# Kernel tuning notes

Measured on AMD Instinct MI355X. Metric: run time of the kernel, lower is better.

Reference implementation:

```python
import jax, jax.numpy as jnp
import numpy as np

B, N, C, H = 2, 2048, 256, 8
HD = C // H
EPS = 1e-5


def _cdist(a, b):
    # a: (B,N,D), b: (B,M,D) -> (B,N,M) euclidean distance (torch.cdist p=2)
    d2 = (jnp.sum(a * a, -1)[:, :, None] + jnp.sum(b * b, -1)[:, None, :]
          - 2.0 * jnp.einsum('bnd,bmd->bnm', a, b))
    return jnp.sqrt(jnp.maximum(d2, 0.0))


def _ln(x, g, b):
    # LayerNorm over last axis
    m = jnp.mean(x, -1, keepdims=True)
    v = jnp.var(x, -1, keepdims=True)
    return (x - m) / jnp.sqrt(v + EPS) * g + b


def _conv1d(x, w, b=None):
    # 1x1 Conv1d: x (B,Cin,N), w (Cout,Cin)
    y = jnp.einsum('oc,bcn->bon', w, x)
    return y if b is None else y + b[:, None]


def setup_inputs() -> dict:
    key = jax.random.key(0)
    ks = jax.random.split(key, 32)
    s = 0.05
    inp = {
        'xyz_A': jax.random.normal(ks[0], (B, N, 3), jnp.float32),
        'featA': jax.random.normal(ks[1], (B, C, N), jnp.float32),
        'xyz_B': jax.random.normal(ks[2], (B, N, 3), jnp.float32),
        'featB': jax.random.normal(ks[3], (B, C, N), jnp.float32),
        # q/k/v projections (Conv1d 1x1)
        'qw': jax.random.normal(ks[4], (C, C), jnp.float32) * s,
        'qb': jnp.zeros((C,), jnp.float32),
        'kw': jax.random.normal(ks[5], (C, C), jnp.float32) * s,
        'kb': jnp.zeros((C,), jnp.float32),
        'vw': jax.random.normal(ks[6], (C, C), jnp.float32) * s,
        'vb': jnp.zeros((C,), jnp.float32),
        # spatial_bias_mlp: Conv2d(1,H/2,1,bias=False) -> BN2d(eval) -> ReLU -> Conv2d(H/2,H,1)
        'sbw1': jax.random.normal(ks[7], (H // 2,), jnp.float32) * s,
        'sbg': jnp.ones((H // 2,), jnp.float32),
        'sbb': jnp.zeros((H // 2,), jnp.float32),
        'sbm': jax.random.normal(ks[8], (H // 2,), jnp.float32) * 0.1,
        'sbv': jax.random.uniform(ks[9], (H // 2,), jnp.float32, 0.5, 1.5),
        'sbw2': jax.random.normal(ks[10], (H, H // 2), jnp.float32) * s,
        'sbb2': jnp.zeros((H,), jnp.float32),
        # dissimilarity projections
        'qdw': jax.random.normal(ks[11], (C, C), jnp.float32) * s,
        'qdb': jnp.zeros((C,), jnp.float32),
        'kdw': jax.random.normal(ks[12], (C, C), jnp.float32) * s,
        'kdb': jnp.zeros((C,), jnp.float32),
        # LayerNorms
        'lin_g': jnp.ones((C,), jnp.float32), 'lin_b': jnp.zeros((C,), jnp.float32),
        'lsim_g': jnp.ones((C,), jnp.float32), 'lsim_b': jnp.zeros((C,), jnp.float32),
        'ldis_g': jnp.ones((C,), jnp.float32), 'ldis_b': jnp.zeros((C,), jnp.float32),
        # fusion MLP: Conv1d(3C,2C,bias=False) -> BN1d(eval) -> ReLU -> Dropout(eval) -> Conv1d(2C,C)
        'fw1': jax.random.normal(ks[13], (2 * C, 3 * C), jnp.float32) * s,
        'fbg': jnp.ones((2 * C,), jnp.float32),
        'fbb': jnp.zeros((2 * C,), jnp.float32),
        'fbm': jax.random.normal(ks[14], (2 * C,), jnp.float32) * 0.1,
        'fbv': jax.random.uniform(ks[15], (2 * C,), jnp.float32, 0.5, 1.5),
        'fw2': jax.random.normal(ks[16], (C, 2 * C), jnp.float32) * s,
        'fb2': jnp.zeros((C,), jnp.float32),
    }
    return inp


def _forward(xyz_A, featA, xyz_B, featB, qw, qb, kw, kb, vw, vb,
             sbw1, sbg, sbb, sbm, sbv, sbw2, sbb2,
             qdw, qdb, kdw, kdb,
             lin_g, lin_b, lsim_g, lsim_b, ldis_g, ldis_b,
             fw1, fbg, fbb, fbm, fbv, fw2, fb2):
    # Pre-norm of featA over channels
    featA_norm = _ln(featA.transpose(0, 2, 1), lin_g, lin_b).transpose(0, 2, 1)  # (B,C,N)

    # Spatial bias: -cdist -> 1x1 conv (in_ch=1) -> BN(eval) -> ReLU -> 1x1 conv
    dist = _cdist(xyz_A, xyz_B)                                # (B,N,N)
    t = jnp.einsum('o,bnm->bonm', sbw1, -dist)                 # (B,H/2,N,N)
    t = (t - sbm[:, None, None]) / jnp.sqrt(sbv + EPS)[:, None, None]
    t = t * sbg[:, None, None] + sbb[:, None, None]
    t = jax.nn.relu(t)
    spatial_bias = jnp.einsum('oh,bhnm->bonm', sbw2, t) + sbb2[:, None, None]  # (B,H,N,N)

    # Similarity path
    q = _conv1d(featA_norm, qw, qb).reshape(B, H, HD, N).transpose(0, 1, 3, 2)  # (B,H,N,hd)
    k = _conv1d(featB, kw, kb).reshape(B, H, HD, N).transpose(0, 1, 3, 2)
    sim_scores = jnp.einsum('bhnd,bhmd->bhnm', q, k) / (HD ** 0.5) + spatial_bias

    # Dissimilarity path: feature cdist + spatial bias
    qd = _conv1d(featA_norm, qdw, qdb).transpose(0, 2, 1)      # (B,N,C)
    kd = _conv1d(featB, kdw, kdb).transpose(0, 2, 1)
    dissim_scores = _cdist(qd, kd)[:, None] + spatial_bias     # (B,H,N,N)

    sim_w = jax.nn.softmax(sim_scores, -1)
    dis_w = jax.nn.softmax(dissim_scores, -1)

    v = _conv1d(featB, vw, vb).reshape(B, H, HD, N).transpose(0, 1, 3, 2)       # (B,H,N,hd)
    ctx_sim = jnp.einsum('bhnm,bhmd->bhnd', sim_w, v).transpose(0, 1, 3, 2).reshape(B, C, N)
    ctx_sim = _ln(ctx_sim.transpose(0, 2, 1), lsim_g, lsim_b).transpose(0, 2, 1)
    ctx_dis = jnp.einsum('bhnm,bhmd->bhnd', dis_w, v).transpose(0, 1, 3, 2).reshape(B, C, N)
    ctx_dis = _ln(ctx_dis.transpose(0, 2, 1), ldis_g, ldis_b).transpose(0, 2, 1)

    fused = jnp.concatenate([featA_norm, ctx_sim, ctx_dis], axis=1)            # (B,3C,N)
    x = jnp.einsum('oc,bcn->bon', fw1, fused)
    x = (x - fbm[:, None]) / jnp.sqrt(fbv + EPS)[:, None] * fbg[:, None] + fbb[:, None]
    x = jax.nn.relu(x)  # Dropout is identity in eval mode
    out = _conv1d(x, fw2, fb2) + featA  # residual_proj is Identity (in==out)
    return out


def reference(xyz_A, featA, xyz_B, featB, qw, qb, kw, kb, vw, vb,
              sbw1, sbg, sbb, sbm, sbv, sbw2, sbb2,
              qdw, qdb, kdw, kdb,
              lin_g, lin_b, lsim_g, lsim_b, ldis_g, ldis_b,
              fw1, fbg, fbb, fbm, fbv, fw2, fb2):
    return _forward(xyz_A, featA, xyz_B, featB, qw, qb, kw, kb, vw, vb,
                    sbw1, sbg, sbb, sbm, sbv, sbw2, sbb2,
                    qdw, qdb, kdw, kdb,
                    lin_g, lin_b, lsim_g, lsim_b, ldis_g, ldis_b,
                    fw1, fbg, fbb, fbm, fbv, fw2, fb2)
```

## Files before the change

kernel.cpp:

```cpp
#include <hip/hip_runtime.h>

#define B_ 2
#define N_ 2048
#define C_ 256
#define H_ 8
#define HD_ 32
#define EPSf 1e-5f
#define LOG2E 1.4426950408889634f
#define THRv 8.0f

typedef __bf16   bf16x8 __attribute__((ext_vector_type(8)));
typedef float    f32x4  __attribute__((ext_vector_type(4)));
typedef _Float16 f16x4  __attribute__((ext_vector_type(4)));
typedef _Float16 f16x2  __attribute__((ext_vector_type(2)));

static constexpr size_t MB_ = 1024 * 1024;
static constexpr size_t OFF_FANT = 0;
static constexpr size_t OFF_FBT  = 2 * MB_;
static constexpr size_t OFF_QPK  = 4 * MB_;
static constexpr size_t OFF_KPK  = 6 * MB_;
static constexpr size_t OFF_VPK  = 8 * MB_;
static constexpr size_t OFF_QDT  = 10 * MB_;
static constexpr size_t OFF_KDT  = 12 * MB_;
static constexpr size_t OFF_QQ   = 14 * MB_;
static constexpr size_t OFF_KK   = 14 * MB_ + 16 * 1024;
static constexpr size_t OFF_FSD  = 14 * MB_ + 64 * 1024;
static constexpr size_t OFF_PART  = 47 * MB_;
static constexpr size_t OFF_STATM = 55 * MB_;
static constexpr size_t OFF_STATL = 56 * MB_;
static constexpr size_t OFF_CSLN  = 15 * MB_;
static constexpr size_t OFF_CDLN  = 17 * MB_;
static constexpr size_t OFF_X1T   = 19 * MB_;
static constexpr size_t WS_NEED   = 63 * MB_;

__device__ __forceinline__ float rfl(float x){
  return __uint_as_float(__builtin_amdgcn_readfirstlane(__float_as_uint(x)));
}
__device__ __forceinline__ float fexp2(float x){ return __builtin_amdgcn_exp2f(x); }
__device__ __forceinline__ bf16x8 cvt8(const float* p){
  float4 a = *reinterpret_cast<const float4*>(p);
  float4 c = *reinterpret_cast<const float4*>(p + 4);
  bf16x8 r;
  r[0]=(__bf16)a.x; r[1]=(__bf16)a.y; r[2]=(__bf16)a.z; r[3]=(__bf16)a.w;
  r[4]=(__bf16)c.x; r[5]=(__bf16)c.y; r[6]=(__bf16)c.z; r[7]=(__bf16)c.w;
  return r;
}
__device__ __forceinline__ unsigned int packh2(float lo, float hi){
  f16x2 h; h[0] = (_Float16)lo; h[1] = (_Float16)hi;
  return __builtin_bit_cast(unsigned int, h);
}
__device__ __forceinline__ void unpackh2(unsigned int u, float& lo, float& hi){
  f16x2 h = __builtin_bit_cast(f16x2, u);
  lo = (float)h[0]; hi = (float)h[1];
}
__device__ __forceinline__ f16x4 pack4(float a, float b, float c, float d){
  auto lo = __builtin_amdgcn_cvt_pkrtz(a, b);
  auto hi = __builtin_amdgcn_cvt_pkrtz(c, d);
  unsigned long long u = (unsigned long long)__builtin_bit_cast(unsigned int, lo)
      | ((unsigned long long)__builtin_bit_cast(unsigned int, hi) << 32);
  return __builtin_bit_cast(f16x4, u);
}

__global__ __launch_bounds__(256) void prep_kernel(const float* __restrict__ featA,
    const float* __restrict__ featB, __bf16* __restrict__ fanT, __bf16* __restrict__ fbT,
    const float* __restrict__ gam, const float* __restrict__ bet){
  int b = blockIdx.y;
  int t = threadIdx.x;
  __shared__ float sh[9536];
  if (blockIdx.x < 64){
    int n0 = blockIdx.x * 32;
    int nl = t & 31, cg = t >> 5;
    float* tile = sh;
    float* red1 = sh + 8448;
    float* red2 = red1 + 256;
    float* mus  = red2 + 256;
    float* rss  = mus + 32;
    float* gsh  = rss + 32;
    float* bsh  = gsh + 256;
    gsh[t] = gam[t]; bsh[t] = bet[t];
    #pragma unroll
    for (int i = 0; i < 32; i++){
      int c = cg * 32 + i;
      tile[c * 33 + nl] = featA[((size_t)(b * C_ + c)) * N_ + n0 + nl];
    }
    __syncthreads();
    float s1 = 0.f, s2 = 0.f;
    #pragma unroll
    for (int i = 0; i < 32; i++){
      float v = tile[(cg * 32 + i) * 33 + nl];
      s1 += v; s2 += v * v;
    }
    red1[cg * 32 + nl] = s1; red2[cg * 32 + nl] = s2;
    __syncthreads();
    if (t < 32){
      float a = 0.f, q = 0.f;
      #pragma unroll
      for (int i = 0; i < 8; i++){ a += red1[i * 32 + t]; q += red2[i * 32 + t]; }
      float m = a / (float)C_;
      mus[t] = m; rss[t] = rsqrtf(q / (float)C_ - m * m + EPSf);
    }
    __syncthreads();
    float mu = mus[nl], rs = rss[nl];
    size_t obase = ((size_t)(b * N_ + n0 + nl)) * C_;
    #pragma unroll
    for (int i = 0; i < 32; i++){
      int c = cg * 32 + i;
      fanT[obase + c] = (__bf16)((tile[c * 33 + nl] - mu) * rs * gsh[c] + bsh[c]);
    }
  } else {
    int idx = blockIdx.x - 64;
    int n0 = (idx & 31) * 64, c0 = (idx >> 5) * 64;
    float* tile = sh;
    int cl = t >> 6, nl = t & 63;
    #pragma unroll
    for (int i = 0; i < 16; i++)
      tile[(i * 4 + cl) * 65 + nl] = featB[((size_t)(b * C_ + c0 + i * 4 + cl)) * N_ + n0 + nl];
    __syncthreads();
    int nr = t >> 2, cc = (t & 3) * 16;
    alignas(16) __bf16 tmp[16];
    #pragma unroll
    for (int j = 0; j < 16; j++) tmp[j] = (__bf16)tile[(cc + j) * 65 + nr];
    size_t d = ((size_t)(b * N_ + n0 + nr)) * C_ + c0 + cc;
    *reinterpret_cast<uint4*>(&fbT[d])     = *reinterpret_cast<uint4*>(&tmp[0]);
    *reinterpret_cast<uint4*>(&fbT[d + 8]) = *reinterpret_cast<uint4*>(&tmp[8]);
  }
}

__global__ __launch_bounds__(256) void proj_mfma(const __bf16* __restrict__ fanT,
    const __bf16* __restrict__ fbT, __bf16* __restrict__ wsh,
    const float* __restrict__ qw, const float* __restrict__ qb,
    const float* __restrict__ kw, const float* __restrict__ kb,
    const float* __restrict__ vw, const float* __restrict__ vb,
    const float* __restrict__ qdw, const float* __restrict__ qdb,
    const float* __restrict__ kdw, const float* __restrict__ kdb){
  const int p = blockIdx.z % 5, b = blockIdx.z / 5;
  const int t = threadIdx.x, w = t >> 6, lane = t & 63, ln = lane & 15, g = lane >> 4;
  const float *W, *bias;
  const __bf16* X;
  __bf16* Y;
  if (p == 0)      { W = qw;  bias = qb;  X = fanT; Y = wsh + (OFF_QPK - OFF_FANT) / 2; }
  else if (p == 1) { W = kw;  bias = kb;  X = fbT;  Y = wsh + (OFF_KPK - OFF_FANT) / 2; }
  else if (p == 2) { W = vw;  bias = vb;  X = fbT;  Y = wsh + (OFF_VPK - OFF_FANT) / 2; }
  else if (p == 3) { W = qdw; bias = qdb; X = fanT; Y = wsh + (OFF_QDT - OFF_FANT) / 2; }
  else             { W = kdw; bias = kdb; X = fbT;  Y = wsh + (OFF_KDT - OFF_FANT) / 2; }

  f32x4 acc[4];
  #pragma unroll
  for (int i = 0; i < 4; i++) acc[i] = (f32x4){0.f, 0.f, 0.f, 0.f};

  if (p != 2){
    const int n0w = blockIdx.x * 64 + w * 16, o0 = blockIdx.y * 64;
    #pragma unroll
    for (int ks = 0; ks < 8; ks++){
      bf16x8 af = *reinterpret_cast<const bf16x8*>(
          &X[((size_t)(b * N_ + n0w + ln)) * C_ + ks * 32 + g * 8]);
      #pragma unroll
      for (int ot = 0; ot < 4; ot++){
        bf16x8 bf = cvt8(&W[(size_t)(o0 + ot * 16 + ln) * C_ + ks * 32 + g * 8]);
        acc[ot] = __builtin_amdgcn_mfma_f32_16x16x32_bf16(af, bf, acc[ot], 0, 0, 0);
      }
    }
    const float inv = 0.17677669529663687f * LOG2E;
    #pragma unroll
    for (int ot = 0; ot < 4; ot++){
      int o = o0 + ot * 16 + ln;
      float bz = bias[o];
      #pragma unroll
      for (int r = 0; r < 4; r++){
        int n = n0w + g * 4 + r;
        float val = acc[ot][r] + bz;
        if (p == 0){
          val *= inv;
          Y[(((size_t)(b * H_ + (o >> 5))) * N_ + n) * HD_ + (o & 31)] = (__bf16)val;
        } else if (p == 1){
          Y[(((size_t)(b * H_ + (o >> 5))) * N_ + n) * HD_ + (o & 31)] = (__bf16)val;
        } else {
          Y[((size_t)(b * N_ + n)) * C_ + o] = (__bf16)val;
        }
      }
    }
  } else {
    const int o0w = blockIdx.y * 64 + w * 16, n0 = blockIdx.x * 64;
    #pragma unroll
    for (int ks = 0; ks < 8; ks++){
      bf16x8 af = cvt8(&W[(size_t)(o0w + ln) * C_ + ks * 32 + g * 8]);
      #pragma unroll
      for (int nt = 0; nt < 4; nt++){
        bf16x8 bf = *reinterpret_cast<const bf16x8*>(
            &X[((size_t)(b * N_ + n0 + nt * 16 + ln)) * C_ + ks * 32 + g * 8]);
        acc[nt] = __builtin_amdgcn_mfma_f32_16x16x32_bf16(af, bf, acc[nt], 0, 0, 0);
      }
    }
    float bz[4];
    #pragma unroll
    for (int r = 0; r < 4; r++) bz[r] = vb[o0w + g * 4 + r];
    #pragma unroll
    for (int nt = 0; nt < 4; nt++)
      #pragma unroll
      for (int r = 0; r < 4; r++){
        int o = o0w + g * 4 + r, n = n0 + nt * 16 + ln;
        size_t idx = ((size_t)(b * C_ + o)) * N_ + n;
        ((_Float16*)Y)[idx] = (_Float16)(acc[nt][r] + bz[r]);
      }
  }
}

__global__ __launch_bounds__(256) void norms_b(const __bf16* __restrict__ qdT,
    const __bf16* __restrict__ kdT, float* __restrict__ qq, float* __restrict__ kk){
  int b = blockIdx.y, n = blockIdx.x * 64 + (threadIdx.x >> 2), part = threadIdx.x & 3;
  size_t base = ((size_t)(b * N_ + n)) * C_ + part * 64;
  float s1 = 0.f, s2 = 0.f;
  #pragma unroll
  for (int i = 0; i < 8; i++){
    bf16x8 a = *reinterpret_cast<const bf16x8*>(&qdT[base + i * 8]);
    bf16x8 d = *reinterpret_cast<const bf16x8*>(&kdT[base + i * 8]);
    #pragma unroll
    for (int j = 0; j < 8; j++){
      float fa = (float)a[j]; s1 += fa * fa;
      float fd = (float)d[j]; s2 += fd * fd;
    }
  }
  s1 += __shfl_xor(s1, 1); s1 += __shfl_xor(s1, 2);
  s2 += __shfl_xor(s2, 1); s2 += __shfl_xor(s2, 2);
  if (part == 0){ qq[b * N_ + n] = s1; kk[b * N_ + n] = s2; }
}

__global__ __launch_bounds__(256) void pairdist_mfma(const __bf16* __restrict__ qdT,
    const __bf16* __restrict__ kdT, const float* __restrict__ qq,
    const float* __restrict__ kk, const float* __restrict__ xyzA,
    const float* __restrict__ xyzB, unsigned int* __restrict__ fsd){
  const int t = threadIdx.x, w = t >> 6, lane = t & 63, ln = lane & 15, g = lane >> 4;
  const int b = blockIdx.z, n0 = blockIdx.y * 64, n0w = n0 + w * 16, m0 = blockIdx.x * 64;
  __shared__ float4 xa[64], xb[64];
  __shared__ unsigned int sbl[4][16][68];

  if (t < 64){
    const float* p = &xyzA[((size_t)(b * N_ + n0 + t)) * 3];
    xa[t] = make_float4(p[0], p[1], p[2], 0.f);
  } else if (t < 128){
    const float* p = &xyzB[((size_t)(b * N_ + m0 + t - 64)) * 3];
    xb[t - 64] = make_float4(p[0], p[1], p[2], 0.f);
  }
  bf16x8 qfr[8];
  #pragma unroll
  for (int ks = 0; ks < 8; ks++)
    qfr[ks] = *reinterpret_cast<const bf16x8*>(
        &qdT[((size_t)(b * N_ + n0w + ln)) * C_ + ks * 32 + g * 8]);
  float qqv[4];
  #pragma unroll
  for (int r = 0; r < 4; r++) qqv[r] = qq[b * N_ + n0w + g * 4 + r];
  __syncthreads();
  float4 xav[4];
  #pragma unroll
  for (int r = 0; r < 4; r++) xav[r] = xa[w * 16 + g * 4 + r];

  #pragma unroll
  for (int mt = 0; mt < 4; mt++){
    f32x4 a = (f32x4){0.f, 0.f, 0.f, 0.f};
    #pragma unroll
    for (int ks = 0; ks < 8; ks++){
      bf16x8 kfr = *reinterpret_cast<const bf16x8*>(
          &kdT[((size_t)(b * N_ + m0 + mt * 16 + ln)) * C_ + ks * 32 + g * 8]);
      a = __builtin_amdgcn_mfma_f32_16x16x32_bf16(qfr[ks], kfr, a, 0, 0, 0);
    }
    float kkv = kk[b * N_ + m0 + mt * 16 + ln];
    float4 xbv = xb[mt * 16 + ln];
    #pragma unroll
    for (int r = 0; r < 4; r++){
      float d2 = qqv[r] + kkv - 2.f * a[r];
      float fd = sqrtf(fmaxf(d2, 0.f)) * LOG2E;
      float dx = xav[r].x - xbv.x, dy = xav[r].y - xbv.y, dz = xav[r].z - xbv.z;
      float sd = sqrtf(dx * dx + dy * dy + dz * dz);
      sbl[w][g * 4 + r][mt * 16 + ln] = packh2(fd, sd);
    }
  }
  #pragma unroll
  for (int it = 0; it < 4; it++){
    int row = it * 4 + (lane >> 4), cq = lane & 15;
    uint4 v = *reinterpret_cast<const uint4*>(&sbl[w][row][cq * 4]);
    *reinterpret_cast<uint4*>(&fsd[((size_t)(b * N_ + n0w + row)) * N_ + m0 + cq * 4]) = v;
  }
}

struct TileRegs { uint4 fu[4]; bf16x8 kf[4]; };

__device__ __forceinline__ void load_tile(TileRegs& T, const __bf16* kbase,
    const unsigned int* fsdrow, int m0, int ln, int g){
  #pragma unroll
  for (int mt = 0; mt < 4; mt++){
    T.fu[mt] = *reinterpret_cast<const uint4*>(&fsdrow[m0 + mt * 16 + g * 4]);
    T.kf[mt] = *reinterpret_cast<const bf16x8*>(&kbase[(size_t)(m0 + mt * 16 + ln) * HD_ + g * 8]);
  }
}

__device__ __forceinline__ void compute_tile4(const TileRegs& T,
    const _Float16* vbase, int m0, int ln, int g, bf16x8 qf,
    const float* Ac, const float* Bc, const float* W2h, float C0,
    f32x4* os, f32x4* od, float& ms, float& lps, float& md, float& lpd){
  f32x4 sa[4];
  #pragma unroll
  for (int mt = 0; mt < 4; mt++){
    f32x4 z = (f32x4){0.f, 0.f, 0.f, 0.f};
    sa[mt] = __builtin_amdgcn_mfma_f32_16x16x32_bf16(T.kf[mt], qf, z, 0, 0, 0);
  }
  f16x4 vf[2][4];
  #pragma unroll
  for (int mt = 0; mt < 4; mt++)
    #pragma unroll
    for (int dt = 0; dt < 2; dt++)
      vf[dt][mt] = *reinterpret_cast<const f16x4*>(
          &vbase[(size_t)(dt * 16 + ln) * N_ + m0 + mt * 16 + g * 4]);
  f32x4 dvv[4];
  float mxs = -3e38f, mxd = -3e38f;
  #pragma unroll
  for (int mt = 0; mt < 4; mt++){
    #pragma unroll
    for (int r = 0; r < 4; r++){
      unsigned int uu = (r == 0) ? T.fu[mt].x : (r == 1) ? T.fu[mt].y
                      : (r == 2) ? T.fu[mt].z : T.fu[mt].w;
      float fdl, sd;
      unpackh2(uu, fdl, sd);
      float u0 = fmaxf(fmaf(Ac[0], sd, Bc[0]), 0.f);
      float u1 = fmaxf(fmaf(Ac[1], sd, Bc[1]), 0.f);
      float u2 = fmaxf(fmaf(Ac[2], sd, Bc[2]), 0.f);
      float u3 = fmaxf(fmaf(Ac[3], sd, Bc[3]), 0.f);
      float bias = fmaf(W2h[0], u0, fmaf(W2h[1], u1, fmaf(W2h[2], u2, fmaf(W2h[3], u3, C0))));
      float s = sa[mt][r] + bias;
      float d = fdl + bias;
      sa[mt][r] = s; dvv[mt][r] = d;
      mxs = fmaxf(mxs, s); mxd = fmaxf(mxd, d);
    }
  }
  if (!__all(mxs <= ms + THRv)){
    float mr = fmaxf(mxs, __shfl_xor(mxs, 16));
    mr = fmaxf(mr, __shfl_xor(mr, 32));
    float nms = fmaxf(ms, mr);
    float als = fexp2(ms - nms);
    ms = nms; lps *= als;
    float a0 = __shfl(als, g * 4 + 0), a1 = __shfl(als, g * 4 + 1);
    float a2 = __shfl(als, g * 4 + 2), a3 = __shfl(als, g * 4 + 3);
    #pragma unroll
    for (int dt = 0; dt < 2; dt++){
      os[dt][0] *= a0; os[dt][1] *= a1; os[dt][2] *= a2; os[dt][3] *= a3;
    }
  }
  if (!__all(mxd <= md + THRv)){
    float mr = fmaxf(mxd, __shfl_xor(mxd, 16));
    mr = fmaxf(mr, __shfl_xor(mr, 32));
    float nmd = fmaxf(md, mr);
    float ald = fexp2(md - nmd);
    md = nmd; lpd *= ald;
    float a0 = __shfl(ald, g * 4 + 0), a1 = __shfl(ald, g * 4 + 1);
    float a2 = __shfl(ald, g * 4 + 2), a3 = __shfl(ald, g * 4 + 3);
    #pragma unroll
    for (int dt = 0; dt < 2; dt++){
      od[dt][0] *= a0; od[dt][1] *= a1; od[dt][2] *= a2; od[dt][3] *= a3;
    }
  }
  f16x4 pAs[4], pAd[4];
  #pragma unroll
  for (int mt = 0; mt < 4; mt++){
    float p0 = fexp2(sa[mt][0] - ms), p1 = fexp2(sa[mt][1] - ms);
    float p2 = fexp2(sa[mt][2] - ms), p3 = fexp2(sa[mt][3] - ms);
    lps += (p0 + p1) + (p2 + p3);
    pAs[mt] = pack4(p0, p1, p2, p3);
    float q0 = fexp2(dvv[mt][0] - md), q1 = fexp2(dvv[mt][1] - md);
    float q2 = fexp2(dvv[mt][2] - md), q3 = fexp2(dvv[mt][3] - md);
    lpd += (q0 + q1) + (q2 + q3);
    pAd[mt] = pack4(q0, q1, q2, q3);
  }
  #pragma unroll
  for (int mt = 0; mt < 4; mt++)
    #pragma unroll
    for (int dt = 0; dt < 2; dt++){
      os[dt] = __builtin_amdgcn_mfma_f32_16x16x16f16(pAs[mt], vf[dt][mt], os[dt], 0, 0, 0);
      od[dt] = __builtin_amdgcn_mfma_f32_16x16x16f16(pAd[mt], vf[dt][mt], od[dt], 0, 0, 0);
    }
}

__global__ __launch_bounds__(256) void dual_attn4(
    const __bf16* __restrict__ qpk, const __bf16* __restrict__ kpk,
    const _Float16* __restrict__ vph, const unsigned int* __restrict__ fsd,
    const float* __restrict__ sbw1, const float* __restrict__ sbg, const float* __restrict__ sbb,
    const float* __restrict__ sbm, const float* __restrict__ sbv,
    const float* __restrict__ sbw2, const float* __restrict__ sbb2,
    _Float16* __restrict__ partO, float* __restrict__ statM, float* __restrict__ statL){
  const int t = threadIdx.x, w = t >> 6, lane = t & 63, ln = lane & 15, g = lane >> 4;
  const int h = blockIdx.y;
  const int b = blockIdx.z >> 1, split = blockIdx.z & 1;
  const int nbase = blockIdx.x * 64 + w * 16;
  const int n = nbase + ln;
  const int mstart = split * (N_ / 2);

  float Ac[4], Bc[4], W2h[4];
  #pragma unroll
  for (int j = 0; j < 4; j++){
    float rs = rsqrtf(sbv[j] + EPSf);
    Ac[j]  = rfl(-sbw1[j] * rs * sbg[j]);
    Bc[j]  = rfl(-sbm[j] * rs * sbg[j] + sbb[j]);
    W2h[j] = rfl(sbw2[h * 4 + j]) * LOG2E;
  }
  float C0 = rfl(sbb2[h]) * LOG2E;

  bf16x8 qf = *reinterpret_cast<const bf16x8*>(
      &qpk[(((size_t)(b * H_ + h)) * N_ + n) * HD_ + g * 8]);
  const unsigned int* fsdrow = &fsd[((size_t)(b * N_ + n)) * N_];
  const __bf16* kbase = &kpk[(((size_t)(b * H_ + h)) * N_) * HD_];
  const _Float16* vbase = &vph[((size_t)(b * C_ + h * HD_)) * N_];

  f32x4 os[2], od[2];
  #pragma unroll
  for (int i = 0; i < 2; i++){ os[i] = (f32x4){0.f,0.f,0.f,0.f}; od[i] = (f32x4){0.f,0.f,0.f,0.f}; }
  float ms = -3e38f, lps = 0.f, md = -3e38f, lpd = 0.f;

  TileRegs TA, TB;
  load_tile(TA, kbase, fsdrow, mstart, ln, g);
  for (int i = 0; i < 16; i += 2){
    int m0 = mstart + i * 64;
    load_tile(TB, kbase, fsdrow, m0 + 64, ln, g);
    compute_tile4(TA, vbase, m0, ln, g, qf, Ac, Bc, W2h, C0, os, od, ms, lps, md, lpd);
    if (i + 2 < 16) load_tile(TA, kbase, fsdrow, m0 + 128, ln, g);
    compute_tile4(TB, vbase, m0 + 64, ln, g, qf, Ac, Bc, W2h, C0, os, od, ms, lps, md, lpd);
  }

  lps += __shfl_xor(lps, 16); lps += __shfl_xor(lps, 32);
  lpd += __shfl_xor(lpd, 16); lpd += __shfl_xor(lpd, 32);
  float is = 1.f / lps, idd = 1.f / lpd;
  float isr[4], idr[4];
  #pragma unroll
  for (int r = 0; r < 4; r++){
    isr[r] = __shfl(is, g * 4 + r);
    idr[r] = __shfl(idd, g * 4 + r);
  }
  #pragma unroll
  for (int dt = 0; dt < 2; dt++)
    #pragma unroll
    for (int r = 0; r < 4; r++){
      int nn = nbase + g * 4 + r;
      int ch = h * HD_ + dt * 16 + ln;
      size_t p0 = (((size_t)(0 * 2 + split) * B_ + b) * N_ + nn) * C_ + ch;
      size_t p1 = (((size_t)(2 + split) * B_ + b) * N_ + nn) * C_ + ch;
      partO[p0] = (_Float16)(os[dt][r] * isr[r]);
      partO[p1] = (_Float16)(od[dt][r] * idr[r]);
    }
  if (lane < 16){
    int nn = nbase + lane;
    size_t s0 = (((size_t)(0 * 2 + split) * B_ + b) * H_ + h) * N_ + nn;
    size_t s1 = (((size_t)(2 + split) * B_ + b) * H_ + h) * N_ + nn;
    statM[s0] = ms; statL[s0] = lps;
    statM[s1] = md; statL[s1] = lpd;
  }
}

__global__ __launch_bounds__(256) void combine_ln(
    const _Float16* __restrict__ partO, const float* __restrict__ statM,
    const float* __restrict__ statL, __bf16* __restrict__ csLN, __bf16* __restrict__ cdLN,
    const float* __restrict__ lsg, const float* __restrict__ lsb,
    const float* __restrict__ ldg, const float* __restrict__ ldb){
  const int path = blockIdx.y;
  const int w = threadIdx.x >> 6, lane = threadIdx.x & 63;
  const size_t row = (size_t)blockIdx.x * 4 + w;
  const int b = (int)(row >> 11), n = (int)(row & (N_ - 1));
  const int h = lane >> 3;
  const float* gg = path ? ldg : lsg;
  const float* bb = path ? ldb : lsb;
  __bf16* dst = path ? cdLN : csLN;

  size_t pb0 = (((size_t)(path * 2 + 0) * B_ + b) * N_ + n) * C_ + lane * 4;
  size_t pb1 = (((size_t)(path * 2 + 1) * B_ + b) * N_ + n) * C_ + lane * 4;
  f16x4 p0 = *reinterpret_cast<const f16x4*>(&partO[pb0]);
  f16x4 p1 = *reinterpret_cast<const f16x4*>(&partO[pb1]);
  size_t sb0 = (((size_t)(path * 2 + 0) * B_ + b) * H_ + h) * N_ + n;
  size_t sb1 = (((size_t)(path * 2 + 1) * B_ + b) * H_ + h) * N_ + n;
  float m0 = statM[sb0], l0 = statL[sb0];
  float m1 = statM[sb1], l1 = statL[sb1];
  float M = fmaxf(m0, m1);
  float w0 = l0 * fexp2(m0 - M), w1 = l1 * fexp2(m1 - M);
  float inv = 1.f / (w0 + w1);
  float o[4];
  #pragma unroll
  for (int j = 0; j < 4; j++)
    o[j] = (w0 * (float)p0[j] + w1 * (float)p1[j]) * inv;

  float s1 = o[0] + o[1] + o[2] + o[3];
  float s2 = o[0]*o[0] + o[1]*o[1] + o[2]*o[2] + o[3]*o[3];
  #pragma unroll
  for (int off = 1; off < 64; off <<= 1){
    s1 += __shfl_xor(s1, off);
    s2 += __shfl_xor(s2, off);
  }
  float mu = s1 / (float)C_;
  float rs = rsqrtf(s2 / (float)C_ - mu * mu + EPSf);
  float4 g4 = *reinterpret_cast<const float4*>(&gg[lane * 4]);
  float4 b4 = *reinterpret_cast<const float4*>(&bb[lane * 4]);
  alignas(8) __bf16 o4[4];
  o4[0] = (__bf16)((o[0] - mu) * rs * g4.x + b4.x);
  o4[1] = (__bf16)((o[1] - mu) * rs * g4.y + b4.y);
  o4[2] = (__bf16)((o[2] - mu) * rs * g4.z + b4.z);
  o4[3] = (__bf16)((o[3] - mu) * rs * g4.w + b4.w);
  *reinterpret_cast<uint2*>(&dst[row * C_ + lane * 4]) = *reinterpret_cast<uint2*>(o4);
}

__global__ __launch_bounds__(256) void fusion1_mfma(const __bf16* __restrict__ fanT,
    const __bf16* __restrict__ csLN, const __bf16* __restrict__ cdLN,
    __bf16* __restrict__ X1T, const float* __restrict__ fw1,
    const float* __restrict__ fbg, const float* __restrict__ fbb,
    const float* __restrict__ fbm, const float* __restrict__ fbv){
  const int t = threadIdx.x, w = t >> 6, lane = t & 63, ln = lane & 15, g = lane >> 4;
  const int b = blockIdx.z, o0 = blockIdx.y * 64, n0w = blockIdx.x * 64 + w * 16;
  f32x4 acc[4];
  #pragma unroll
  for (int i = 0; i < 4; i++) acc[i] = (f32x4){0.f, 0.f, 0.f, 0.f};
  const __bf16* segs[3] = {fanT, csLN, cdLN};
  #pragma unroll
  for (int ks = 0; ks < 24; ks++){
    const __bf16* base = segs[ks >> 3];
    int coff = (ks & 7) * 32 + g * 8;
    bf16x8 af = *reinterpret_cast<const bf16x8*>(
        &base[((size_t)(b * N_ + n0w + ln)) * C_ + coff]);
    #pragma unroll
    for (int ot = 0; ot < 4; ot++){
      bf16x8 bf = cvt8(&fw1[(size_t)(o0 + ot * 16 + ln) * (3 * C_) + ks * 32 + g * 8]);
      acc[ot] = __builtin_amdgcn_mfma_f32_16x16x32_bf16(af, bf, acc[ot], 0, 0, 0);
    }
  }
  #pragma unroll
  for (int ot = 0; ot < 4; ot++){
    int o = o0 + ot * 16 + ln;
    float mn = fbm[o], rs = rsqrtf(fbv[o] + EPSf), gg = fbg[o], be = fbb[o];
    #pragma unroll
    for (int r = 0; r < 4; r++){
      int n = n0w + g * 4 + r;
      float x = (acc[ot][r] - mn) * rs * gg + be;
      X1T[((size_t)(b * N_ + n)) * (2 * C_) + o] = (__bf16)fmaxf(x, 0.f);
    }
  }
}

__global__ __launch_bounds__(256) void fusion2_mfma(const __bf16* __restrict__ X1T,
    const float* __restrict__ fw2, const float* __restrict__ fb2,
    const float* __restrict__ featA, float* __restrict__ out){
  const int t = threadIdx.x, w = t >> 6, lane = t & 63, ln = lane & 15, g = lane >> 4;
  const int b = blockIdx.z, o0w = blockIdx.y * 64 + w * 16, n0 = blockIdx.x * 64;
  f32x4 acc[4];
  #pragma unroll
  for (int i = 0; i < 4; i++) acc[i] = (f32x4){0.f, 0.f, 0.f, 0.f};
  #pragma unroll
  for (int ks = 0; ks < 16; ks++){
    bf16x8 af = cvt8(&fw2[(size_t)(o0w + ln) * (2 * C_) + ks * 32 + g * 8]);
    #pragma unroll
    for (int nt = 0; nt < 4; nt++){
      bf16x8 bf = *reinterpret_cast<const bf16x8*>(
          &X1T[((size_t)(b * N_ + n0 + nt * 16 + ln)) * (2 * C_) + ks * 32 + g * 8]);
      acc[nt] = __builtin_amdgcn_mfma_f32_16x16x32_bf16(af, bf, acc[nt], 0, 0, 0);
    }
  }
  float bz[4];
  #pragma unroll
  for (int r = 0; r < 4; r++) bz[r] = fb2[o0w + g * 4 + r];
  #pragma unroll
  for (int nt = 0; nt < 4; nt++)
    #pragma unroll
    for (int r = 0; r < 4; r++){
      int o = o0w + g * 4 + r, n = n0 + nt * 16 + ln;
      size_t oi = ((size_t)(b * C_ + o)) * N_ + n;
      out[oi] = acc[nt][r] + bz[r] + featA[oi];
    }
}

extern "C" void kernel_launch(void* const* d_in, const int* in_sizes, int n_in,
                              void* d_out, int out_size, void* d_ws, size_t ws_size,
                              hipStream_t stream){
  (void)in_sizes; (void)n_in; (void)out_size;
  if (ws_size < WS_NEED) return;

  const float* xyzA  = (const float*)d_in[0];
  const float* featA = (const float*)d_in[1];
  const float* xyzB  = (const float*)d_in[2];
  const float* featB = (const float*)d_in[3];
  const float* qw  = (const float*)d_in[4];   const float* qb  = (const float*)d_in[5];
  const float* kw  = (const float*)d_in[6];   const float* kb  = (const float*)d_in[7];
  const float* vw  = (const float*)d_in[8];   const float* vb  = (const float*)d_in[9];
  const float* sbw1= (const float*)d_in[10];  const float* sbg = (const float*)d_in[11];
  const float* sbb = (const float*)d_in[12];  const float* sbm = (const float*)d_in[13];
  const float* sbv = (const float*)d_in[14];  const float* sbw2= (const float*)d_in[15];
  const float* sbb2= (const float*)d_in[16];
  const float* qdw = (const float*)d_in[17];  const float* qdb = (const float*)d_in[18];
  const float* kdw = (const float*)d_in[19];  const float* kdb = (const float*)d_in[20];
  const float* ling= (const float*)d_in[21];  const float* linb= (const float*)d_in[22];
  const float* lsg = (const float*)d_in[23];  const float* lsb = (const float*)d_in[24];
  const float* ldg = (const float*)d_in[25];  const float* ldb = (const float*)d_in[26];
  const float* fw1 = (const float*)d_in[27];  const float* fbg = (const float*)d_in[28];
  const float* fbb = (const float*)d_in[29];  const float* fbm = (const float*)d_in[30];
  const float* fbv = (const float*)d_in[31];  const float* fw2 = (const float*)d_in[32];
  const float* fb2 = (const float*)d_in[33];

  char* ws = (char*)d_ws;
  __bf16*   fanT = (__bf16*)(ws + OFF_FANT);
  __bf16*   fbT  = (__bf16*)(ws + OFF_FBT);
  __bf16*   qpk  = (__bf16*)(ws + OFF_QPK);
  __bf16*   kpk  = (__bf16*)(ws + OFF_KPK);
  _Float16* vph  = (_Float16*)(ws + OFF_VPK);
  __bf16*   qdT  = (__bf16*)(ws + OFF_QDT);
  __bf16*   kdT  = (__bf16*)(ws + OFF_KDT);
  float*    qq   = (float*)(ws + OFF_QQ);
  float*    kk   = (float*)(ws + OFF_KK);
  unsigned int* fsd = (unsigned int*)(ws + OFF_FSD);
  _Float16* partO = (_Float16*)(ws + OFF_PART);
  float*    statM = (float*)(ws + OFF_STATM);
  float*    statL = (float*)(ws + OFF_STATL);
  __bf16*   csLN  = (__bf16*)(ws + OFF_CSLN);
  __bf16*   cdLN  = (__bf16*)(ws + OFF_CDLN);
  __bf16*   X1T   = (__bf16*)(ws + OFF_X1T);
  float*    out   = (float*)d_out;

  prep_kernel<<<dim3(192, B_), 256, 0, stream>>>(featA, featB, fanT, fbT, ling, linb);
  proj_mfma<<<dim3(N_ / 64, C_ / 64, 5 * B_), 256, 0, stream>>>(
      fanT, fbT, fanT, qw, qb, kw, kb, vw, vb, qdw, qdb, kdw, kdb);
  norms_b<<<dim3(N_ / 64, B_), 256, 0, stream>>>(qdT, kdT, qq, kk);
  pairdist_mfma<<<dim3(N_ / 64, N_ / 64, B_), 256, 0, stream>>>(
      qdT, kdT, qq, kk, xyzA, xyzB, fsd);
  dual_attn4<<<dim3(N_ / 64, H_, B_ * 2), 256, 0, stream>>>(
      qpk, kpk, vph, fsd, sbw1, sbg, sbb, sbm, sbv, sbw2, sbb2,
      partO, statM, statL);
  combine_ln<<<dim3(B_ * N_ / 4, 2), 256, 0, stream>>>(
      partO, statM, statL, csLN, cdLN, lsg, lsb, ldg, ldb);
  fusion1_mfma<<<dim3(N_ / 64, (2 * C_) / 64, B_), 256, 0, stream>>>(
      fanT, csLN, cdLN, X1T, fw1, fbg, fbb, fbm, fbv);
  fusion2_mfma<<<dim3(N_ / 64, C_ / 64, B_), 256, 0, stream>>>(
      X1T, fw2, fb2, featA, out);
}
```

Before: 265.9 us.

## Compute softmax exponentials before max check and launch single-wave attention blocks

```diff
diff --git a/kernel.cpp b/kernel.cpp
--- a/kernel.cpp
+++ b/kernel.cpp
@@ -293,7 +293,7 @@
   }
 }
 
-__device__ __forceinline__ void compute_tile4(const TileRegs& T,
+__device__ __forceinline__ void compute_tile5(const TileRegs& T,
     const _Float16* vbase, int m0, int ln, int g, bf16x8 qf,
     const float* Ac, const float* Bc, const float* W2h, float C0,
     f32x4* os, f32x4* od, float& ms, float& lps, float& md, float& lpd){
@@ -311,7 +311,6 @@
       vf[dt][mt] = *reinterpret_cast<const f16x4*>(
           &vbase[(size_t)(dt * 16 + ln) * N_ + m0 + mt * 16 + g * 4]);
   f32x4 dvv[4];
-  float mxs = -3e38f, mxd = -3e38f;
   #pragma unroll
   for (int mt = 0; mt < 4; mt++){
     #pragma unroll
@@ -325,50 +324,79 @@
       float u2 = fmaxf(fmaf(Ac[2], sd, Bc[2]), 0.f);
       float u3 = fmaxf(fmaf(Ac[3], sd, Bc[3]), 0.f);
       float bias = fmaf(W2h[0], u0, fmaf(W2h[1], u1, fmaf(W2h[2], u2, fmaf(W2h[3], u3, C0))));
-      float s = sa[mt][r] + bias;
-      float d = fdl + bias;
-      sa[mt][r] = s; dvv[mt][r] = d;
-      mxs = fmaxf(mxs, s); mxd = fmaxf(mxd, d);
-    }
+      sa[mt][r] = sa[mt][r] + bias;
+      dvv[mt][r] = fdl + bias;
+    }
+  }
+  f16x4 pAs[4], pAd[4];
+  float tss = 0.f, tsd = 0.f;
+  #pragma unroll
+  for (int mt = 0; mt < 4; mt++){
+    float p0 = fexp2(fminf(sa[mt][0] - ms, 80.f)), p1 = fexp2(fminf(sa[mt][1] - ms, 80.f));
+    float p2 = fexp2(fminf(sa[mt][2] - ms, 80.f)), p3 = fexp2(fminf(sa[mt][3] - ms, 80.f));
+    tss += (p0 + p1) + (p2 + p3);
+    pAs[mt] = pack4(p0, p1, p2, p3);
+    float q0 = fexp2(fminf(dvv[mt][0] - md, 80.f)), q1 = fexp2(fminf(dvv[mt][1] - md, 80.f));
+    float q2 = fexp2(fminf(dvv[mt][2] - md, 80.f)), q3 = fexp2(fminf(dvv[mt][3] - md, 80.f));
+    tsd += (q0 + q1) + (q2 + q3);
+    pAd[mt] = pack4(q0, q1, q2, q3);
+  }
+  float mxs, mxd;
+  {
+    float a0 = fmaxf(fmaxf(sa[0][0], sa[0][1]), fmaxf(sa[0][2], sa[0][3]));
+    float a1 = fmaxf(fmaxf(sa[1][0], sa[1][1]), fmaxf(sa[1][2], sa[1][3]));
+    float a2 = fmaxf(fmaxf(sa[2][0], sa[2][1]), fmaxf(sa[2][2], sa[2][3]));
+    float a3 = fmaxf(fmaxf(sa[3][0], sa[3][1]), fmaxf(sa[3][2], sa[3][3]));
+    mxs = fmaxf(fmaxf(a0, a1), fmaxf(a2, a3));
+    float b0 = fmaxf(fmaxf(dvv[0][0], dvv[0][1]), fmaxf(dvv[0][2], dvv[0][3]));
+    float b1 = fmaxf(fmaxf(dvv[1][0], dvv[1][1]), fmaxf(dvv[1][2], dvv[1][3]));
+    float b2 = fmaxf(fmaxf(dvv[2][0], dvv[2][1]), fmaxf(dvv[2][2], dvv[2][3]));
+    float b3 = fmaxf(fmaxf(dvv[3][0], dvv[3][1]), fmaxf(dvv[3][2], dvv[3][3]));
+    mxd = fmaxf(fmaxf(b0, b1), fmaxf(b2, b3));
   }
   if (!__all(mxs <= ms + THRv)){
     float mr = fmaxf(mxs, __shfl_xor(mxs, 16));
     mr = fmaxf(mr, __shfl_xor(mr, 32));
     float nms = fmaxf(ms, mr);
-    float als = fexp2(ms - nms);
-    ms = nms; lps *= als;
-    float a0 = __shfl(als, g * 4 + 0), a1 = __shfl(als, g * 4 + 1);
-    float a2 = __shfl(als, g * 4 + 2), a3 = __shfl(als, g * 4 + 3);
+    float f = fexp2(ms - nms);
+    ms = nms; lps *= f;
+    float a0 = __shfl(f, g * 4 + 0), a1 = __shfl(f, g * 4 + 1);
+    float a2 = __shfl(f, g * 4 + 2), a3 = __shfl(f, g * 4 + 3);
     #pragma unroll
     for (int dt = 0; dt < 2; dt++){
       os[dt][0] *= a0; os[dt][1] *= a1; os[dt][2] *= a2; os[dt][3] *= a3;
+    }
+    tss = 0.f;
+    #pragma unroll
+    for (int mt = 0; mt < 4; mt++){
+      float p0 = fexp2(sa[mt][0] - ms), p1 = fexp2(sa[mt][1] - ms);
+      float p2 = fexp2(sa[mt][2] - ms), p3 = fexp2(sa[mt][3] - ms);
+      tss += (p0 + p1) + (p2 + p3);
+      pAs[mt] = pack4(p0, p1, p2, p3);
     }
   }
   if (!__all(mxd <= md + THRv)){
     float mr = fmaxf(mxd, __shfl_xor(mxd, 16));
     mr = fmaxf(mr, __shfl_xor(mr, 32));
     float nmd = fmaxf(md, mr);
-    float ald = fexp2(md - nmd);
-    md = nmd; lpd *= ald;
-    float a0 = __shfl(ald, g * 4 + 0), a1 = __shfl(ald, g * 4 + 1);
-    float a2 = __shfl(ald, g * 4 + 2), a3 = __shfl(ald, g * 4 + 3);
+    float f = fexp2(md - nmd);
+    md = nmd; lpd *= f;
+    float a0 = __shfl(f, g * 4 + 0), a1 = __shfl(f, g * 4 + 1);
+    float a2 = __shfl(f, g * 4 + 2), a3 = __shfl(f, g * 4 + 3);
     #pragma unroll
     for (int dt = 0; dt < 2; dt++){
       od[dt][0] *= a0; od[dt][1] *= a1; od[dt][2] *= a2; od[dt][3] *= a3;
     }
-  }
-  f16x4 pAs[4], pAd[4];
-  #pragma unroll
-  for (int mt = 0; mt < 4; mt++){
-    float p0 = fexp2(sa[mt][0] - ms), p1 = fexp2(sa[mt][1] - ms);
-    float p2 = fexp2(sa[mt][2] - ms), p3 = fexp2(sa[mt][3] - ms);
-    lps += (p0 + p1) + (p2 + p3);
-    pAs[mt] = pack4(p0, p1, p2, p3);
-    float q0 = fexp2(dvv[mt][0] - md), q1 = fexp2(dvv[mt][1] - md);
-    float q2 = fexp2(dvv[mt][2] - md), q3 = fexp2(dvv[mt][3] - md);
-    lpd += (q0 + q1) + (q2 + q3);
-    pAd[mt] = pack4(q0, q1, q2, q3);
-  }
+    tsd = 0.f;
+    #pragma unroll
+    for (int mt = 0; mt < 4; mt++){
+      float q0 = fexp2(dvv[mt][0] - md), q1 = fexp2(dvv[mt][1] - md);
+      float q2 = fexp2(dvv[mt][2] - md), q3 = fexp2(dvv[mt][3] - md);
+      tsd += (q0 + q1) + (q2 + q3);
+      pAd[mt] = pack4(q0, q1, q2, q3);
+    }
+  }
+  lps += tss; lpd += tsd;
   #pragma unroll
   for (int mt = 0; mt < 4; mt++)
     #pragma unroll
@@ -378,17 +406,17 @@
     }
 }
 
-__global__ __launch_bounds__(256) void dual_attn4(
+__global__ __launch_bounds__(64, 4) void dual_attn5(
     const __bf16* __restrict__ qpk, const __bf16* __restrict__ kpk,
     const _Float16* __restrict__ vph, const unsigned int* __restrict__ fsd,
     const float* __restrict__ sbw1, const float* __restrict__ sbg, const float* __restrict__ sbb,
     const float* __restrict__ sbm, const float* __restrict__ sbv,
     const float* __restrict__ sbw2, const float* __restrict__ sbb2,
     _Float16* __restrict__ partO, float* __restrict__ statM, float* __restrict__ statL){
-  const int t = threadIdx.x, w = t >> 6, lane = t & 63, ln = lane & 15, g = lane >> 4;
+  const int lane = threadIdx.x, ln = lane & 15, g = lane >> 4;
   const int h = blockIdx.y;
   const int b = blockIdx.z >> 1, split = blockIdx.z & 1;
-  const int nbase = blockIdx.x * 64 + w * 16;
+  const int nbase = blockIdx.x * 16;
   const int n = nbase + ln;
   const int mstart = split * (N_ / 2);
 
@@ -418,9 +446,9 @@
   for (int i = 0; i < 16; i += 2){
     int m0 = mstart + i * 64;
     load_tile(TB, kbase, fsdrow, m0 + 64, ln, g);
-    compute_tile4(TA, vbase, m0, ln, g, qf, Ac, Bc, W2h, C0, os, od, ms, lps, md, lpd);
+    compute_tile5(TA, vbase, m0, ln, g, qf, Ac, Bc, W2h, C0, os, od, ms, lps, md, lpd);
     if (i + 2 < 16) load_tile(TA, kbase, fsdrow, m0 + 128, ln, g);
-    compute_tile4(TB, vbase, m0 + 64, ln, g, qf, Ac, Bc, W2h, C0, os, od, ms, lps, md, lpd);
+    compute_tile5(TB, vbase, m0 + 64, ln, g, qf, Ac, Bc, W2h, C0, os, od, ms, lps, md, lpd);
   }
 
   lps += __shfl_xor(lps, 16); lps += __shfl_xor(lps, 32);
@@ -620,7 +648,7 @@
   norms_b<<<dim3(N_ / 64, B_), 256, 0, stream>>>(qdT, kdT, qq, kk);
   pairdist_mfma<<<dim3(N_ / 64, N_ / 64, B_), 256, 0, stream>>>(
       qdT, kdT, qq, kk, xyzA, xyzB, fsd);
-  dual_attn4<<<dim3(N_ / 64, H_, B_ * 2), 256, 0, stream>>>(
+  dual_attn5<<<dim3(N_ / 16, H_, B_ * 2), 64, 0, stream>>>(
       qpk, kpk, vph, fsd, sbw1, sbg, sbb, sbm, sbv, sbw2, sbb2,
       partO, statM, statL);
   combine_ln<<<dim3(B_ * N_ / 4, 2), 256, 0, stream>>>(
```

After: 323.9 us. 1.22x slower.

## Compute softmax exps speculatively with old max, drop double-buffered tile loads

Applied to the files above, without the earlier changes.

```diff
diff --git a/kernel.cpp b/kernel.cpp
--- a/kernel.cpp
+++ b/kernel.cpp
@@ -293,7 +293,7 @@
   }
 }
 
-__device__ __forceinline__ void compute_tile4(const TileRegs& T,
+__device__ __forceinline__ void compute_tile7(const TileRegs& T,
     const _Float16* vbase, int m0, int ln, int g, bf16x8 qf,
     const float* Ac, const float* Bc, const float* W2h, float C0,
     f32x4* os, f32x4* od, float& ms, float& lps, float& md, float& lpd){
@@ -310,10 +310,11 @@
     for (int dt = 0; dt < 2; dt++)
       vf[dt][mt] = *reinterpret_cast<const f16x4*>(
           &vbase[(size_t)(dt * 16 + ln) * N_ + m0 + mt * 16 + g * 4]);
-  f32x4 dvv[4];
-  float mxs = -3e38f, mxd = -3e38f;
+  f16x4 pAs[4], pAd[4];
+  float tss = 0.f, tsd = 0.f, mxs = -3e38f, mxd = -3e38f;
   #pragma unroll
   for (int mt = 0; mt < 4; mt++){
+    float ps[4], pd[4];
     #pragma unroll
     for (int r = 0; r < 4; r++){
       unsigned int uu = (r == 0) ? T.fu[mt].x : (r == 1) ? T.fu[mt].y
@@ -327,48 +328,67 @@
       float bias = fmaf(W2h[0], u0, fmaf(W2h[1], u1, fmaf(W2h[2], u2, fmaf(W2h[3], u3, C0))));
       float s = sa[mt][r] + bias;
       float d = fdl + bias;
-      sa[mt][r] = s; dvv[mt][r] = d;
       mxs = fmaxf(mxs, s); mxd = fmaxf(mxd, d);
-    }
-  }
-  if (!__all(mxs <= ms + THRv)){
-    float mr = fmaxf(mxs, __shfl_xor(mxs, 16));
-    mr = fmaxf(mr, __shfl_xor(mr, 32));
-    float nms = fmaxf(ms, mr);
-    float als = fexp2(ms - nms);
-    ms = nms; lps *= als;
-    float a0 = __shfl(als, g * 4 + 0), a1 = __shfl(als, g * 4 + 1);
-    float a2 = __shfl(als, g * 4 + 2), a3 = __shfl(als, g * 4 + 3);
-    #pragma unroll
-    for (int dt = 0; dt < 2; dt++){
-      os[dt][0] *= a0; os[dt][1] *= a1; os[dt][2] *= a2; os[dt][3] *= a3;
-    }
-  }
-  if (!__all(mxd <= md + THRv)){
-    float mr = fmaxf(mxd, __shfl_xor(mxd, 16));
-    mr = fmaxf(mr, __shfl_xor(mr, 32));
-    float nmd = fmaxf(md, mr);
-    float ald = fexp2(md - nmd);
-    md = nmd; lpd *= ald;
-    float a0 = __shfl(ald, g * 4 + 0), a1 = __shfl(ald, g * 4 + 1);
-    float a2 = __shfl(ald, g * 4 + 2), a3 = __shfl(ald, g * 4 + 3);
-    #pragma unroll
-    for (int dt = 0; dt < 2; dt++){
-      od[dt][0] *= a0; od[dt][1] *= a1; od[dt][2] *= a2; od[dt][3] *= a3;
-    }
-  }
-  f16x4 pAs[4], pAd[4];
-  #pragma unroll
-  for (int mt = 0; mt < 4; mt++){
-    float p0 = fexp2(sa[mt][0] - ms), p1 = fexp2(sa[mt][1] - ms);
-    float p2 = fexp2(sa[mt][2] - ms), p3 = fexp2(sa[mt][3] - ms);
-    lps += (p0 + p1) + (p2 + p3);
-    pAs[mt] = pack4(p0, p1, p2, p3);
-    float q0 = fexp2(dvv[mt][0] - md), q1 = fexp2(dvv[mt][1] - md);
-    float q2 = fexp2(dvv[mt][2] - md), q3 = fexp2(dvv[mt][3] - md);
-    lpd += (q0 + q1) + (q2 + q3);
-    pAd[mt] = pack4(q0, q1, q2, q3);
-  }
+      ps[r] = fexp2(s - ms); pd[r] = fexp2(d - md);
+      tss += ps[r]; tsd += pd[r];
+    }
+    pAs[mt] = pack4(ps[0], ps[1], ps[2], ps[3]);
+    pAd[mt] = pack4(pd[0], pd[1], pd[2], pd[3]);
+  }
+  bool fs  = !__all(mxs <= ms + THRv);
+  bool fdp = !__all(mxd <= md + THRv);
+  if (fs || fdp){
+    if (fs){
+      float mr = fmaxf(mxs, __shfl_xor(mxs, 16));
+      mr = fmaxf(mr, __shfl_xor(mr, 32));
+      float nms = fmaxf(ms, mr);
+      float f = fexp2(ms - nms);
+      ms = nms; lps *= f;
+      float a0 = __shfl(f, g * 4 + 0), a1 = __shfl(f, g * 4 + 1);
+      float a2 = __shfl(f, g * 4 + 2), a3 = __shfl(f, g * 4 + 3);
+      #pragma unroll
+      for (int dt = 0; dt < 2; dt++){
+        os[dt][0] *= a0; os[dt][1] *= a1; os[dt][2] *= a2; os[dt][3] *= a3;
+      }
+    }
+    if (fdp){
+      float mr = fmaxf(mxd, __shfl_xor(mxd, 16));
+      mr = fmaxf(mr, __shfl_xor(mr, 32));
+      float nmd = fmaxf(md, mr);
+      float f = fexp2(md - nmd);
+      md = nmd; lpd *= f;
+      float a0 = __shfl(f, g * 4 + 0), a1 = __shfl(f, g * 4 + 1);
+      float a2 = __shfl(f, g * 4 + 2), a3 = __shfl(f, g * 4 + 3);
+      #pragma unroll
+      for (int dt = 0; dt < 2; dt++){
+        od[dt][0] *= a0; od[dt][1] *= a1; od[dt][2] *= a2; od[dt][3] *= a3;
+      }
+    }
+    tss = 0.f; tsd = 0.f;
+    #pragma unroll
+    for (int mt = 0; mt < 4; mt++){
+      float ps[4], pd[4];
+      #pragma unroll
+      for (int r = 0; r < 4; r++){
+        unsigned int uu = (r == 0) ? T.fu[mt].x : (r == 1) ? T.fu[mt].y
+                        : (r == 2) ? T.fu[mt].z : T.fu[mt].w;
+        float fdl, sd;
+        unpackh2(uu, fdl, sd);
+        float u0 = fmaxf(fmaf(Ac[0], sd, Bc[0]), 0.f);
+        float u1 = fmaxf(fmaf(Ac[1], sd, Bc[1]), 0.f);
+        float u2 = fmaxf(fmaf(Ac[2], sd, Bc[2]), 0.f);
+        float u3 = fmaxf(fmaf(Ac[3], sd, Bc[3]), 0.f);
+        float bias = fmaf(W2h[0], u0, fmaf(W2h[1], u1, fmaf(W2h[2], u2, fmaf(W2h[3], u3, C0))));
+        float s = sa[mt][r] + bias;
+        float d = fdl + bias;
+        ps[r] = fexp2(s - ms); pd[r] = fexp2(d - md);
+        tss += ps[r]; tsd += pd[r];
+      }
+      pAs[mt] = pack4(ps[0], ps[1], ps[2], ps[3]);
+      pAd[mt] = pack4(pd[0], pd[1], pd[2], pd[3]);
+    }
+  }
+  lps += tss; lpd += tsd;
   #pragma unroll
   for (int mt = 0; mt < 4; mt++)
     #pragma unroll
@@ -378,7 +398,7 @@
     }
 }
 
-__global__ __launch_bounds__(256) void dual_attn4(
+__global__ __launch_bounds__(256, 4) void dual_attn7(
     const __bf16* __restrict__ qpk, const __bf16* __restrict__ kpk,
     const _Float16* __restrict__ vph, const unsigned int* __restrict__ fsd,
     const float* __restrict__ sbw1, const float* __restrict__ sbg, const float* __restrict__ sbb,
@@ -413,14 +433,11 @@
   for (int i = 0; i < 2; i++){ os[i] = (f32x4){0.f,0.f,0.f,0.f}; od[i] = (f32x4){0.f,0.f,0.f,0.f}; }
   float ms = -3e38f, lps = 0.f, md = -3e38f, lpd = 0.f;
 
-  TileRegs TA, TB;
-  load_tile(TA, kbase, fsdrow, mstart, ln, g);
-  for (int i = 0; i < 16; i += 2){
+  TileRegs T;
+  for (int i = 0; i < 16; i++){
     int m0 = mstart + i * 64;
-    load_tile(TB, kbase, fsdrow, m0 + 64, ln, g);
-    compute_tile4(TA, vbase, m0, ln, g, qf, Ac, Bc, W2h, C0, os, od, ms, lps, md, lpd);
-    if (i + 2 < 16) load_tile(TA, kbase, fsdrow, m0 + 128, ln, g);
-    compute_tile4(TB, vbase, m0 + 64, ln, g, qf, Ac, Bc, W2h, C0, os, od, ms, lps, md, lpd);
+    load_tile(T, kbase, fsdrow, m0, ln, g);
+    compute_tile7(T, vbase, m0, ln, g, qf, Ac, Bc, W2h, C0, os, od, ms, lps, md, lpd);
   }
 
   lps += __shfl_xor(lps, 16); lps += __shfl_xor(lps, 32);
@@ -620,7 +637,7 @@
   norms_b<<<dim3(N_ / 64, B_), 256, 0, stream>>>(qdT, kdT, qq, kk);
   pairdist_mfma<<<dim3(N_ / 64, N_ / 64, B_), 256, 0, stream>>>(
       qdT, kdT, qq, kk, xyzA, xyzB, fsd);
-  dual_attn4<<<dim3(N_ / 64, H_, B_ * 2), 256, 0, stream>>>(
+  dual_attn7<<<dim3(N_ / 64, H_, B_ * 2), 256, 0, stream>>>(
       qpk, kpk, vph, fsd, sbw1, sbg, sbb, sbm, sbv, sbw2, sbb2,
       partO, statM, statL);
   combine_ln<<<dim3(B_ * N_ / 4, 2), 256, 0, stream>>>(
```

Result: slower. 282.8 us (+6.3%).
